# Kernel tuning notes

Measured on AMD Instinct MI355X. Metric: run time of the kernel, lower is better.

## Reference

```python
import jax, jax.numpy as jnp
import numpy as np

N = 16384      # instances (cells) per bag
IN = 2000      # input_dim (genes)
E1, E2 = 1024, 512   # encoder_dims
HID = 512      # hidden_dim
NH, HD = 8, 64 # num_heads, head_dim
LK = 256       # linformer_k
EPROJ_N = 10000  # fixed in-dim of E/F projections
NEXP, MH = 4, 256  # moe experts, moe hidden (= classifier_dims[0])
C1, C2, NC = 256, 128, 2


def _ln(x, g, b):
    m = jnp.mean(x, axis=-1, keepdims=True)
    v = jnp.var(x, axis=-1, keepdims=True)
    return (x - m) * jax.lax.rsqrt(v + 1e-5) * g + b


def setup_inputs() -> dict:
    key = jax.random.key(0)
    ks = jax.random.split(key, 24)
    s = 0.02
    f32 = jnp.float32
    inp = {
        'x': jax.random.normal(ks[0], (N, IN), dtype=f32),
        'enc_w1': jax.random.normal(ks[1], (IN, E1), dtype=f32) * s,
        'enc_b1': jnp.zeros((E1,), f32),
        'enc_w2': jax.random.normal(ks[2], (E1, E2), dtype=f32) * s,
        'enc_b2': jnp.zeros((E2,), f32),
        'enc_w3': jax.random.normal(ks[3], (E2, HID), dtype=f32) * s,
        'enc_b3': jnp.zeros((HID,), f32),
        'q_w': jax.random.normal(ks[4], (HID, HID), dtype=f32) * s,
        'q_b': jnp.zeros((HID,), f32),
        'k_w': jax.random.normal(ks[5], (HID, HID), dtype=f32) * s,
        'k_b': jnp.zeros((HID,), f32),
        'v_w': jax.random.normal(ks[6], (HID, HID), dtype=f32) * s,
        'v_b': jnp.zeros((HID,), f32),
        'o_w': jax.random.normal(ks[7], (HID, HID), dtype=f32) * s,
        'o_b': jnp.zeros((HID,), f32),
        'E_w': jax.random.normal(ks[8], (LK, EPROJ_N), dtype=f32) * s,  # nn.Linear(10000, k).weight
        'F_w': jax.random.normal(ks[9], (LK, EPROJ_N), dtype=f32) * s,
        'ln1_g': jnp.ones((HID,), f32), 'ln1_b': jnp.zeros((HID,), f32),
        'ln2_g': jnp.ones((HID,), f32), 'ln2_b': jnp.zeros((HID,), f32),
        'gate_w': jax.random.normal(ks[10], (HID, NEXP), dtype=f32) * s,
        'gate_b': jnp.zeros((NEXP,), f32),
        'moe_w1': jax.random.normal(ks[11], (NEXP, HID, MH), dtype=f32) * s,
        'moe_b1': jnp.zeros((NEXP, MH), f32),
        'moe_w2': jax.random.normal(ks[12], (NEXP, MH), dtype=f32) * s,
        'moe_b2': jnp.zeros((NEXP,), f32),
        'cls_w1': jax.random.normal(ks[13], (HID, C1), dtype=f32) * s,
        'cls_b1': jnp.zeros((C1,), f32),
        'cls_w2': jax.random.normal(ks[14], (C1, C2), dtype=f32) * s,
        'cls_b2': jnp.zeros((C2,), f32),
        'cls_w3': jax.random.normal(ks[15], (C2, NC), dtype=f32) * s,
        'cls_b3': jnp.zeros((NC,), f32),
    }
    return inp


def reference(x, enc_w1, enc_b1, enc_w2, enc_b2, enc_w3, enc_b3,
              q_w, q_b, k_w, k_b, v_w, v_b, o_w, o_b, E_w, F_w,
              ln1_g, ln1_b, ln2_g, ln2_b,
              gate_w, gate_b, moe_w1, moe_b1, moe_w2, moe_b2,
              cls_w1, cls_b1, cls_w2, cls_b2, cls_w3, cls_b3):
    # --- instance encoder (chunking in torch is math-equivalent to one pass) ---
    h = jax.nn.relu(x @ enc_w1 + enc_b1)
    h = jax.nn.relu(h @ enc_w2 + enc_b2)
    feat = jax.nn.relu(h @ enc_w3 + enc_b3)          # [N, HID]
    # dropouts / InstanceDropout are identity at inference

    # --- linformer attention (single bag, batch of 1) ---
    Q = (feat @ q_w + q_b).reshape(N, NH, HD).transpose(1, 0, 2)  # [H, N, D]
    K = (feat @ k_w + k_b).reshape(N, NH, HD).transpose(1, 0, 2)
    V = (feat @ v_w + v_b).reshape(N, NH, HD).transpose(1, 0, 2)
    # N > linformer_k and the torch inner check (seq_len <= weight.size(0)=LK)
    # is false, so E/F are bilinearly resized from [10000, LK] to [LK, N], then
    # transposed to [N, LK] (matches F.interpolate align_corners=False).
    E_m = jax.image.resize(E_w.T, (LK, N), method='bilinear').T   # [N, LK]
    F_m = jax.image.resize(F_w.T, (LK, N), method='bilinear').T   # [N, LK]
    Kc = jnp.einsum('hnd,nk->hkd', K, E_m)           # [H, LK, D]
    Vc = jnp.einsum('hnd,nk->hkd', V, F_m)           # [H, LK, D]
    scores = jax.nn.softmax(jnp.einsum('hnd,hkd->hnk', Q, Kc) * (HD ** -0.5), axis=-1)
    ao = jnp.einsum('hnk,hkd->hnd', scores, Vc)      # [H, N, D]
    attn_out = ao.transpose(1, 0, 2).reshape(N, HID) @ o_w + o_b

    att = _ln(attn_out + feat, ln1_g, ln1_b)
    att = _ln(att, ln2_g, ln2_b)                     # [N, HID]

    # --- MoE MIL aggregation: gated mixture of per-expert attention pooling ---
    gates = jax.nn.softmax(jnp.mean(att, axis=0) @ gate_w + gate_b)       # [E]
    Hm = jnp.tanh(jnp.einsum('nd,edh->enh', att, moe_w1) + moe_b1[:, None, :])
    sc = jnp.einsum('enh,eh->en', Hm, moe_w2) + moe_b2[:, None]           # [E, N]
    a = jax.nn.softmax(sc, axis=1)                   # per-expert instance attention
    attn_weights = gates @ a                         # [N]
    bag = attn_weights @ att                         # [HID]

    # --- classifier ---
    c = jax.nn.relu(bag @ cls_w1 + cls_b1)
    c = jax.nn.relu(c @ cls_w2 + cls_b2)
    disease = c @ cls_w3 + cls_b3                    # [NC]
    # use_domain_adaptation=False -> no domain output
    return (bag, disease, attn_weights)
```

## Files before the change

### kernel.cpp

```cpp
#include <hip/hip_runtime.h>

#define DI __device__ __forceinline__

DI float bf2f(unsigned short u){ unsigned int v = ((unsigned int)u)<<16; float f; __builtin_memcpy(&f,&v,4); return f; }
DI unsigned short f2bf(float f){ unsigned int v; __builtin_memcpy(&v,&f,4); v = v + 0x7FFFu + ((v>>16)&1u); return (unsigned short)(v>>16); }

typedef __attribute__((ext_vector_type(8))) short bf16x8;
typedef __attribute__((ext_vector_type(4))) float f32x4;

#define GLD_LDS16(src, dst) __builtin_amdgcn_global_load_lds( \
    (const __attribute__((address_space(1))) void*)(src), \
    (__attribute__((address_space(3))) void*)(dst), 16, 0, 0)

DI void barrier_() { asm volatile("" ::: "memory"); __builtin_amdgcn_s_barrier(); asm volatile("" ::: "memory"); }

template<int ACT>
__global__ __launch_bounds__(256) void gemm2_k(
    const unsigned short* __restrict__ A, const unsigned short* __restrict__ Bt,
    const float* __restrict__ bias, unsigned short* __restrict__ C,
    int K, int lda, int ldb, int ldc)
{
  __shared__ unsigned short As[8192];
  __shared__ unsigned short Bs[8192];
  const int tid = threadIdx.x, lane = tid & 63, wid = tid >> 6;
  const int wm = wid >> 1, wn = wid & 1;
  const int nx = gridDim.x;
  const int bid = blockIdx.x + nx*blockIdx.y;
  const int cpx = (nx*gridDim.y) >> 3;
  const int wg = (bid & 7)*cpx + (bid >> 3);
  const long long mBase = (long long)(wg / nx) << 7;
  const long long nBase = (long long)(wg % nx) << 7;
  const int q = lane >> 4, r15 = lane & 15;

  f32x4 acc[4][4];
#pragma unroll
  for (int i=0;i<4;i++)
#pragma unroll
    for (int j=0;j<4;j++)
#pragma unroll
      for (int r=0;r<4;r++) acc[i][j][r] = 0.f;

  const int nkt = K >> 6;
  for (int kt=0; kt<nkt; ++kt) {
    const int k0 = kt << 6;
#pragma unroll
    for (int it=0; it<4; ++it) {
      const int dbase = (it<<8) + (wid<<6);
      const int d = dbase + lane;
      const int row = d >> 3, cc = d & 7, sc = cc ^ (row & 7);
      GLD_LDS16(A + (mBase + row)*(long long)lda + k0 + (sc<<3), As + (dbase<<3));
      GLD_LDS16(Bt + (nBase + row)*(long long)ldb + k0 + (sc<<3), Bs + (dbase<<3));
    }
    __syncthreads();
#pragma unroll
    for (int ks=0; ks<2; ++ks) {
      bf16x8 af[4], bfr[4];
#pragma unroll
      for (int mi=0; mi<4; ++mi) {
        const int row = (wm<<6) + (mi<<4) + r15;
        const int ch = ((ks<<2)+q) ^ (row&7);
        af[mi] = *(const bf16x8*)(As + (row<<6) + (ch<<3));
      }
#pragma unroll
      for (int ni=0; ni<4; ++ni) {
        const int col = (wn<<6) + (ni<<4) + r15;
        const int ch = ((ks<<2)+q) ^ (col&7);
        bfr[ni] = *(const bf16x8*)(Bs + (col<<6) + (ch<<3));
      }
#pragma unroll
      for (int mi=0; mi<4; ++mi)
#pragma unroll
        for (int ni=0; ni<4; ++ni)
          acc[mi][ni] = __builtin_amdgcn_mfma_f32_16x16x32_bf16(af[mi], bfr[ni], acc[mi][ni], 0, 0, 0);
    }
    __syncthreads();
  }
#pragma unroll
  for (int ni=0; ni<4; ++ni) {
    const long long n = nBase + (wn<<6) + (ni<<4) + r15;
    const float bval = bias[n];
#pragma unroll
    for (int mi=0; mi<4; ++mi) {
#pragma unroll
      for (int r=0; r<4; ++r) {
        const long long m = mBase + (wm<<6) + (mi<<4) + (q<<2) + r;
        float v = acc[mi][ni][r] + bval;
        if constexpr (ACT==1) v = fmaxf(v, 0.f);
        C[m*(long long)ldc + n] = f2bf(v);
      }
    }
  }
}

template<int ACT, bool MOE>
__global__ __launch_bounds__(512,2) void gemm4_k(
    const unsigned short* __restrict__ A, const unsigned short* __restrict__ Bt,
    const float* __restrict__ bias, unsigned short* __restrict__ C,
    const float* __restrict__ w2, float* __restrict__ scp,
    int K, int lda, int ldb, int ldc)
{
  __shared__ unsigned short As[2][16384];
  __shared__ unsigned short Bs[2][16384];
  const int tid = threadIdx.x, lane = tid & 63, wid = tid >> 6;
  const int wm = wid >> 2, wn = wid & 3;
  const int q = lane >> 4, r15 = lane & 15;
  const int nx = gridDim.x;
  const int bid = blockIdx.x + nx*blockIdx.y;
  const int cpx = (nx*gridDim.y) >> 3;
  const int wg = (bid & 7)*cpx + (bid >> 3);
  const long long mBase = (long long)(wg / nx) << 8;
  const long long nBase = (long long)(wg % nx) << 8;

  f32x4 acc[8][4];
#pragma unroll
  for (int i=0;i<8;i++)
#pragma unroll
    for (int j=0;j<4;j++)
#pragma unroll
      for (int r=0;r<4;r++) acc[i][j][r] = 0.f;

  const int NT = K >> 6;

#define G4_STA(j, nb, kk) { const int d_ = tid + ((j)<<9); const int row_ = d_>>3, c_ = d_&7, sc_ = c_ ^ (row_&7); \
    GLD_LDS16(A + (mBase+row_)*(long long)lda + (kk) + (sc_<<3), &As[nb][d_<<3]); }
#define G4_STB(j, nb, kk) { const int d_ = tid + ((j)<<9); const int row_ = d_>>3, c_ = d_&7, sc_ = c_ ^ (row_&7); \
    GLD_LDS16(Bt + (nBase+row_)*(long long)ldb + (kk) + (sc_<<3), &Bs[nb][d_<<3]); }

  G4_STB(0,0,0); G4_STB(1,0,0); G4_STB(2,0,0); G4_STB(3,0,0);
  G4_STA(0,0,0); G4_STA(2,0,0); G4_STA(1,0,0); G4_STA(3,0,0);

  for (int t=0; t<NT; ++t) {
    const int b = t & 1, nb = b ^ 1;
    const bool more = (t+1 < NT);
    const int k1 = (t+1) << 6;
    bf16x8 aF[8], bL[4], bH[4];

    asm volatile("s_waitcnt vmcnt(2)" ::: "memory");
    barrier_();
#pragma unroll
    for (int mi=0; mi<4; ++mi)
#pragma unroll
      for (int ks=0; ks<2; ++ks) {
        const int row = (wm<<7) + (mi<<4) + r15;
        const int ch = ((ks<<2)+q) ^ (row&7);
        aF[mi*2+ks] = *(const bf16x8*)&As[b][(row<<6) + (ch<<3)];
      }
#pragma unroll
    for (int ni=0; ni<2; ++ni)
#pragma unroll
      for (int ks=0; ks<2; ++ks) {
        const int col = (wn<<6) + (ni<<4) + r15;
        const int ch = ((ks<<2)+q) ^ (col&7);
        bL[ni*2+ks] = *(const bf16x8*)&Bs[b][(col<<6) + (ch<<3)];
      }
    if (more) { G4_STB(0,nb,k1); G4_STB(1,nb,k1); }
    __builtin_amdgcn_s_setprio(1);
#pragma unroll
    for (int mi=0; mi<4; ++mi)
#pragma unroll
      for (int ni=0; ni<2; ++ni)
#pragma unroll
        for (int ks=0; ks<2; ++ks)
          acc[mi][ni] = __builtin_amdgcn_mfma_f32_16x16x32_bf16(aF[mi*2+ks], bL[ni*2+ks], acc[mi][ni], 0,0,0);
    __builtin_amdgcn_s_setprio(0);
    barrier_();

#pragma unroll
    for (int ni=0; ni<2; ++ni)
#pragma unroll
      for (int ks=0; ks<2; ++ks) {
        const int col = (wn<<6) + ((ni+2)<<4) + r15;
        const int ch = ((ks<<2)+q) ^ (col&7);
        bH[ni*2+ks] = *(const bf16x8*)&Bs[b][(col<<6) + (ch<<3)];
      }
    if (more) { G4_STB(2,nb,k1); G4_STB(3,nb,k1); }
    __builtin_amdgcn_s_setprio(1);
#pragma unroll
    for (int mi=0; mi<4; ++mi)
#pragma unroll
      for (int ni=0; ni<2; ++ni)
#pragma unroll
        for (int ks=0; ks<2; ++ks)
          acc[mi][ni+2] = __builtin_amdgcn_mfma_f32_16x16x32_bf16(aF[mi*2+ks], bH[ni*2+ks], acc[mi][ni+2], 0,0,0);
    __builtin_amdgcn_s_setprio(0);
    barrier_();

    if (more) { asm volatile("s_waitcnt vmcnt(4)" ::: "memory"); }
    else      { asm volatile("s_waitcnt vmcnt(0)" ::: "memory"); }
    barrier_();
#pragma unroll
    for (int mi=0; mi<4; ++mi)
#pragma unroll
      for (int ks=0; ks<2; ++ks) {
        const int row = (wm<<7) + ((mi+4)<<4) + r15;
        const int ch = ((ks<<2)+q) ^ (row&7);
        aF[mi*2+ks] = *(const bf16x8*)&As[b][(row<<6) + (ch<<3)];
      }
    if (more) { G4_STA(0,nb,k1); G4_STA(2,nb,k1); }
    __builtin_amdgcn_s_setprio(1);
#pragma unroll
    for (int mi=0; mi<4; ++mi)
#pragma unroll
      for (int ni=0; ni<2; ++ni)
#pragma unroll
        for (int ks=0; ks<2; ++ks)
          acc[mi+4][ni] = __builtin_amdgcn_mfma_f32_16x16x32_bf16(aF[mi*2+ks], bL[ni*2+ks], acc[mi+4][ni], 0,0,0);
    __builtin_amdgcn_s_setprio(0);
    barrier_();

    if (more) { G4_STA(1,nb,k1); G4_STA(3,nb,k1); }
    __builtin_amdgcn_s_setprio(1);
#pragma unroll
    for (int mi=0; mi<4; ++mi)
#pragma unroll
      for (int ni=0; ni<2; ++ni)
#pragma unroll
        for (int ks=0; ks<2; ++ks)
          acc[mi+4][ni+2] = __builtin_amdgcn_mfma_f32_16x16x32_bf16(aF[mi*2+ks], bH[ni*2+ks], acc[mi+4][ni+2], 0,0,0);
    __builtin_amdgcn_s_setprio(0);
    barrier_();
  }
#undef G4_STA
#undef G4_STB

  if constexpr (MOE) {
    const int e = (int)(nBase >> 8);
#pragma unroll
    for (int mi=0; mi<8; ++mi) {
#pragma unroll
      for (int r=0; r<4; ++r) {
        float p = 0.f;
#pragma unroll
        for (int ni=0; ni<4; ++ni) {
          const int n = (int)nBase + (wn<<6) + (ni<<4) + r15;
          const float v = acc[mi][ni][r] + bias[n];
          const float th = 1.f - 2.f/(__expf(2.f*v) + 1.f);
          p += th * w2[n];
        }
        p += __shfl_xor(p,1,64); p += __shfl_xor(p,2,64);
        p += __shfl_xor(p,4,64); p += __shfl_xor(p,8,64);
        if (r15 == 0) {
          const long long m = mBase + (wm<<7) + (mi<<4) + (q<<2) + r;
          atomicAdd(scp + ((long long)e<<14) + m, p);
        }
      }
    }
  } else {
#pragma unroll
    for (int ni=0; ni<4; ++ni) {
      const long long n = nBase + (wn<<6) + (ni<<4) + r15;
      const float bval = bias[n];
#pragma unroll
      for (int mi=0; mi<8; ++mi) {
#pragma unroll
        for (int r=0; r<4; ++r) {
          const long long m = mBase + (wm<<7) + (mi<<4) + (q<<2) + r;
          float v = acc[mi][ni][r] + bval;
          if constexpr (ACT==1) v = fmaxf(v, 0.f);
          C[m*(long long)ldc + n] = f2bf(v);
        }
      }
    }
  }
}

__global__ __launch_bounds__(256) void cvtx_k(const float* __restrict__ x, unsigned short* __restrict__ xb)
{
  const long long id = (long long)blockIdx.x*256 + threadIdx.x;
  const long long row = id >> 8; const int c = (int)(id & 255);
  bf16x8 v;
  if (c < 250) {
    const float* p = x + row*2000 + c*8;
    const float4 f0 = *(const float4*)p, f1 = *(const float4*)(p+4);
    v[0]=(short)f2bf(f0.x); v[1]=(short)f2bf(f0.y); v[2]=(short)f2bf(f0.z); v[3]=(short)f2bf(f0.w);
    v[4]=(short)f2bf(f1.x); v[5]=(short)f2bf(f1.y); v[6]=(short)f2bf(f1.z); v[7]=(short)f2bf(f1.w);
  } else {
#pragma unroll
    for (int j=0;j<8;j++) v[j]=0;
  }
  *(bf16x8*)(xb + (id<<3)) = v;
}

__global__ __launch_bounds__(256) void cvtw_k(const float* __restrict__ B, unsigned short* __restrict__ Bt,
    int K, int N, int Kpad, long long bszi, long long bszo)
{
  __shared__ float tile[64][65];
  const float* Bz = B + (long long)blockIdx.z*bszi;
  unsigned short* Bo = Bt + (long long)blockIdx.z*bszo;
  const int k0 = blockIdx.x<<6, n0 = blockIdx.y<<6;
  const int c = threadIdx.x & 63, rg = threadIdx.x >> 6;
#pragma unroll
  for (int j=0;j<16;j++){
    const int r = (j<<2) + rg;
    const int k = k0 + r;
    tile[r][c] = (k < K) ? Bz[(long long)k*N + n0 + c] : 0.f;
  }
  __syncthreads();
#pragma unroll
  for (int j=0;j<16;j++){
    const int nn = (j<<2) + rg;
    Bo[(long long)(n0+nn)*Kpad + k0 + c] = f2bf(tile[c][nn]);
  }
}

__global__ __launch_bounds__(256) void cvtw5_k(
    const float* __restrict__ s0, const float* __restrict__ s1, const float* __restrict__ s2,
    const float* __restrict__ s3, const float* __restrict__ s4,
    unsigned short* __restrict__ d0, unsigned short* __restrict__ d1, unsigned short* __restrict__ d2,
    unsigned short* __restrict__ d3, unsigned short* __restrict__ d4)
{
  __shared__ float tile[64][65];
  const int z = blockIdx.z;
  const float* Bz = (z==0)?s0:(z==1)?s1:(z==2)?s2:(z==3)?s3:s4;
  unsigned short* Bo = (z==0)?d0:(z==1)?d1:(z==2)?d2:(z==3)?d3:d4;
  const int k0 = blockIdx.x<<6, n0 = blockIdx.y<<6;
  const int c = threadIdx.x & 63, rg = threadIdx.x >> 6;
#pragma unroll
  for (int j=0;j<16;j++){
    const int r = (j<<2) + rg;
    tile[r][c] = Bz[(long long)(k0+r)*512 + n0 + c];
  }
  __syncthreads();
#pragma unroll
  for (int j=0;j<16;j++){
    const int nn = (j<<2) + rg;
    Bo[(long long)(n0+nn)*512 + k0 + c] = f2bf(tile[c][nn]);
  }
}

__global__ __launch_bounds__(256) void t1cat_k(const float* __restrict__ Ew, const float* __restrict__ Fw,
    float* __restrict__ t1, const float* __restrict__ qb, const float* __restrict__ kb,
    const float* __restrict__ vb, float* __restrict__ qkvb)
{
  const int k = blockIdx.x, which = blockIdx.y, c = threadIdx.x;
  if (which == 0 && k < 3) {
    const float* src = (k==0) ? qb : (k==1) ? kb : vb;
    qkvb[k*512 + c]       = src[c];
    qkvb[k*512 + 256 + c] = src[256 + c];
  }
  const float* W = which ? Fw : Ew;
  const float ksc = 39.0625f;
  const float inv = 1.f/39.0625f;
  const float sf = (k + 0.5f)*ksc - 0.5f;
  int ilo = (int)ceilf(sf - ksc); if (ilo < 0) ilo = 0;
  int ihi = (int)floorf(sf + ksc); if (ihi > 9999) ihi = 9999;
  float acc = 0.f, wsum = 0.f;
  for (int i=ilo; i<=ihi; ++i) {
    const float w = 1.f - fabsf(sf - (float)i)*inv;
    if (w > 0.f) { acc += w * W[c*10000 + i]; wsum += w; }
  }
  t1[(which*256 + k)*256 + c] = acc / wsum;
}

__global__ __launch_bounds__(512) void red_k(const unsigned short* __restrict__ qkv,
                                             float* __restrict__ red)
{
  const int c = blockIdx.x, which = blockIdx.y, j = threadIdx.x;
  const unsigned short* X = qkv + (which ? 1024 : 512);
  int nlo = 64*c - 32; if (nlo < 0) nlo = 0;
  int nhi = 64*c + 95; if (nhi > 16383) nhi = 16383;
  float acc = 0.f;
  for (int n=nlo; n<=nhi; ++n) {
    float sf = (n + 0.5f)*0.015625f - 0.5f;
    sf = fminf(fmaxf(sf, 0.f), 255.f);
    const int c0 = (int)sf;
    const float f = sf - (float)c0;
    float w = 0.f;
    if (c == c0) w = 1.f - f;
    else if (c == c0+1) w = f;
    if (w != 0.f) acc += w * bf2f(X[(long long)n*1536 + j]);
  }
  red[(which*256 + c)*512 + j] = acc;
}

__global__ __launch_bounds__(512) void kc_k(const float* __restrict__ t1, const float* __restrict__ red,
                                            unsigned short* __restrict__ Kc, unsigned short* __restrict__ Vct)
{
  const int k = blockIdx.x, which = blockIdx.y, j = threadIdx.x;
  const float* T = t1 + (which*256 + k)*256;
  const float* R = red + which*131072;
  float acc = 0.f;
  for (int c=0; c<256; ++c) acc += T[c] * R[c*512 + j];
  const int h = j >> 6, d = j & 63;
  if (which == 0) Kc [(h<<14) + (k<<6) + d] = f2bf(acc);
  else            Vct[(h<<14) + (d<<8) + k] = f2bf(acc);
}

__global__ __launch_bounds__(256) void attn_k(
    const unsigned short* __restrict__ Qg, const unsigned short* __restrict__ Kc,
    const unsigned short* __restrict__ Vct, unsigned short* __restrict__ ao)
{
  __shared__ unsigned short Ks[16384];
  __shared__ unsigned short Vs[16384];
  __shared__ unsigned short Ps[32768];
  const int h = blockIdx.y;
  const long long mBase = (long long)blockIdx.x << 7;
  const int tid = threadIdx.x, lane = tid & 63, wid = tid >> 6;
  const int q = lane >> 4, r15 = lane & 15;

#pragma unroll
  for (int it=0; it<8; ++it) {
    const int dbase = (it<<8) + (wid<<6);
    const int d = dbase + lane;
    {
      const int row = d >> 3, cc = d & 7, sc = cc ^ (row & 7);
      GLD_LDS16(Kc + (h<<14) + (row<<6) + (sc<<3), Ks + (dbase<<3));
    }
    {
      const int row = d >> 5, cc = d & 31, sc = (cc & 24) | ((cc ^ (row & 7)) & 7);
      GLD_LDS16(Vct + (h<<14) + (row<<8) + (sc<<3), Vs + (dbase<<3));
    }
  }
  __syncthreads();

  f32x4 acc[2][16];
#pragma unroll
  for (int mi=0;mi<2;mi++)
#pragma unroll
    for (int ni=0;ni<16;ni++)
#pragma unroll
      for (int r=0;r<4;r++) acc[mi][ni][r] = 0.f;

#pragma unroll
  for (int ks=0; ks<2; ++ks) {
    bf16x8 af[2];
#pragma unroll
    for (int mi=0; mi<2; ++mi) {
      const long long m = mBase + (wid<<5) + (mi<<4) + r15;
      af[mi] = *(const bf16x8*)(Qg + m*1536 + (h<<6) + (ks<<5) + (q<<3));
    }
#pragma unroll
    for (int ni=0; ni<16; ++ni) {
      const int col = (ni<<4) + r15;
      const int ch = ((ks<<2)+q) ^ (col&7);
      const bf16x8 bv = *(const bf16x8*)(Ks + (col<<6) + (ch<<3));
      acc[0][ni] = __builtin_amdgcn_mfma_f32_16x16x32_bf16(af[0], bv, acc[0][ni], 0,0,0);
      acc[1][ni] = __builtin_amdgcn_mfma_f32_16x16x32_bf16(af[1], bv, acc[1][ni], 0,0,0);
    }
  }

#pragma unroll
  for (int mi=0; mi<2; ++mi) {
#pragma unroll
    for (int r=0; r<4; ++r) {
      float mx = -3.4e38f;
#pragma unroll
      for (int ni=0; ni<16; ++ni) mx = fmaxf(mx, acc[mi][ni][r]);
      mx = fmaxf(mx, __shfl_xor(mx,1,64)); mx = fmaxf(mx, __shfl_xor(mx,2,64));
      mx = fmaxf(mx, __shfl_xor(mx,4,64)); mx = fmaxf(mx, __shfl_xor(mx,8,64));
      float s = 0.f;
#pragma unroll
      for (int ni=0; ni<16; ++ni) {
        const float e = __expf((acc[mi][ni][r] - mx)*0.125f);
        acc[mi][ni][r] = e; s += e;
      }
      s += __shfl_xor(s,1,64); s += __shfl_xor(s,2,64);
      s += __shfl_xor(s,4,64); s += __shfl_xor(s,8,64);
      const float inv = 1.f / s;
      const int row = (wid<<5) + (mi<<4) + (q<<2) + r;
#pragma unroll
      for (int ni=0; ni<16; ++ni) {
        const int col = (ni<<4) + r15;
        const int ch = col >> 3;
        const int chs = (ch & 24) | ((ch ^ (row & 7)) & 7);
        Ps[(row<<8) + (chs<<3) + (col&7)] = f2bf(acc[mi][ni][r]*inv);
      }
    }
  }
  __syncthreads();

  f32x4 o[2][4];
#pragma unroll
  for (int mi=0;mi<2;mi++)
#pragma unroll
    for (int ni=0;ni<4;ni++)
#pragma unroll
      for (int r=0;r<4;r++) o[mi][ni][r] = 0.f;

#pragma unroll
  for (int kk=0; kk<8; ++kk) {
    bf16x8 pa[2];
#pragma unroll
    for (int mi=0; mi<2; ++mi) {
      const int row = (wid<<5) + (mi<<4) + r15;
      const int ch = (kk<<2) + q;
      const int chs = (ch & 24) | ((ch ^ (row & 7)) & 7);
      pa[mi] = *(const bf16x8*)(Ps + (row<<8) + (chs<<3));
    }
#pragma unroll
    for (int ni=0; ni<4; ++ni) {
      const int vrow = (ni<<4) + r15;
      const int ch = (kk<<2) + q;
      const int chs = (ch & 24) | ((ch ^ (vrow & 7)) & 7);
      const bf16x8 bv = *(const bf16x8*)(Vs + (vrow<<8) + (chs<<3));
      o[0][ni] = __builtin_amdgcn_mfma_f32_16x16x32_bf16(pa[0], bv, o[0][ni], 0,0,0);
      o[1][ni] = __builtin_amdgcn_mfma_f32_16x16x32_bf16(pa[1], bv, o[1][ni], 0,0,0);
    }
  }
#pragma unroll
  for (int mi=0; mi<2; ++mi)
#pragma unroll
    for (int ni=0; ni<4; ++ni)
#pragma unroll
      for (int r=0; r<4; ++r) {
        const long long m = mBase + (wid<<5) + (mi<<4) + (q<<2) + r;
        ao[m*512 + (h<<6) + (ni<<4) + r15] = f2bf(o[mi][ni][r]);
      }
}

__global__ __launch_bounds__(256) void ln2_k(
    const unsigned short* __restrict__ x1b, const unsigned short* __restrict__ x2b,
    const float* __restrict__ g1, const float* __restrict__ b1,
    const float* __restrict__ g2, const float* __restrict__ b2,
    unsigned short* __restrict__ out)
{
  __shared__ float sred[8];
  const int tid = threadIdx.x, lane = tid & 63, wid = tid >> 6;
  const long long base = (long long)blockIdx.x << 9;
  const float x0 = bf2f(x1b[base+tid])     + bf2f(x2b[base+tid]);
  const float x1 = bf2f(x1b[base+256+tid]) + bf2f(x2b[base+256+tid]);
  float s = x0+x1, qq = x0*x0 + x1*x1;
#pragma unroll
  for (int o=32;o;o>>=1){ s += __shfl_xor(s,o,64); qq += __shfl_xor(qq,o,64); }
  if (lane==0){ sred[wid]=s; sred[4+wid]=qq; }
  __syncthreads();
  float mean = (sred[0]+sred[1]+sred[2]+sred[3]) * (1.f/512.f);
  float var  = (sred[4]+sred[5]+sred[6]+sred[7]) * (1.f/512.f) - mean*mean;
  float rs = rsqrtf(var + 1e-5f);
  const float y0 = (x0-mean)*rs*g1[tid]     + b1[tid];
  const float y1 = (x1-mean)*rs*g1[tid+256] + b1[tid+256];
  __syncthreads();
  s = y0+y1; qq = y0*y0 + y1*y1;
#pragma unroll
  for (int o=32;o;o>>=1){ s += __shfl_xor(s,o,64); qq += __shfl_xor(qq,o,64); }
  if (lane==0){ sred[wid]=s; sred[4+wid]=qq; }
  __syncthreads();
  mean = (sred[0]+sred[1]+sred[2]+sred[3]) * (1.f/512.f);
  var  = (sred[4]+sred[5]+sred[6]+sred[7]) * (1.f/512.f) - mean*mean;
  rs = rsqrtf(var + 1e-5f);
  out[base+tid]     = f2bf((y0-mean)*rs*g2[tid]     + b2[tid]);
  out[base+256+tid] = f2bf((y1-mean)*rs*g2[tid+256] + b2[tid+256]);
}

__global__ __launch_bounds__(256) void wcolsum_k(const unsigned short* __restrict__ att,
                                                 float* __restrict__ part, float* __restrict__ zf)
{
  const int c = threadIdx.x;
  if (zf) { zf[((long long)blockIdx.x<<9)+c] = 0.f; zf[((long long)blockIdx.x<<9)+c+256] = 0.f; }
  const long long r0 = (long long)blockIdx.x * 128;
  float a0=0.f, a1=0.f;
  for (int r=0;r<128;r++){
    const unsigned short* p = att + ((r0+r)<<9);
    a0 += bf2f(p[c]); a1 += bf2f(p[c+256]);
  }
  part[((long long)blockIdx.x<<9)+c]     = a0;
  part[((long long)blockIdx.x<<9)+c+256] = a1;
}

__global__ __launch_bounds__(512) void meangates_k(const float* __restrict__ part,
    const float* __restrict__ gw, const float* __restrict__ gb, float* __restrict__ gates)
{
  __shared__ float mv[512];
  __shared__ float tmp[4];
  const int t = threadIdx.x;
  float s = 0.f;
  for (int b=0;b<128;b++) s += part[(b<<9)+t];
  mv[t] = s * (1.f/16384.f);
  __syncthreads();
  if (t < 4) {
    float a = gb[t];
    for (int d=0; d<512; ++d) a += mv[d]*gw[d*4+t];
    tmp[t] = a;
  }
  __syncthreads();
  if (t == 0) {
    const float m = fmaxf(fmaxf(tmp[0],tmp[1]),fmaxf(tmp[2],tmp[3]));
    float e[4]; float ss=0.f;
    for (int i=0;i<4;i++){ e[i]=__expf(tmp[i]-m); ss+=e[i]; }
    for (int i=0;i<4;i++) gates[i] = e[i]/ss;
  }
}

__global__ __launch_bounds__(1024) void moestat_k(const float* __restrict__ sc,
                                                  float* __restrict__ mstat, float* __restrict__ sstat)
{
  __shared__ float red[1024];
  const int e = blockIdx.x, t = threadIdx.x;
  const float* p = sc + e*16384;
  float m = -3.4e38f;
  for (int n=t; n<16384; n+=1024) m = fmaxf(m, p[n]);
  red[t] = m; __syncthreads();
  for (int o=512;o;o>>=1){ if (t<o) red[t]=fmaxf(red[t],red[t+o]); __syncthreads(); }
  m = red[0]; __syncthreads();
  float s = 0.f;
  for (int n=t; n<16384; n+=1024) s += __expf(p[n]-m);
  red[t] = s; __syncthreads();
  for (int o=512;o;o>>=1){ if (t<o) red[t]+=red[t+o]; __syncthreads(); }
  if (t==0){ mstat[e]=m; sstat[e]=red[0]; }
}

__global__ __launch_bounds__(256) void wbag_k(const unsigned short* __restrict__ att,
    const float* __restrict__ scp, const float* __restrict__ gates,
    const float* __restrict__ mstat, const float* __restrict__ sstat,
    float* __restrict__ part, float* __restrict__ dout)
{
  __shared__ float wrow[128];
  const int c = threadIdx.x;
  const long long r0 = (long long)blockIdx.x * 128;
  if (c < 128) {
    const long long n = r0 + c;
    float w = 0.f;
#pragma unroll
    for (int e=0;e<4;e++) w += gates[e]*__expf(scp[((long long)e<<14)+n]-mstat[e]) / sstat[e];
    wrow[c] = w;
    dout[514 + n] = w;
  }
  __syncthreads();
  float a0=0.f, a1=0.f;
  for (int r=0;r<128;r++){
    const float w = wrow[r];
    const unsigned short* p = att + ((r0+r)<<9);
    a0 += w*bf2f(p[c]); a1 += w*bf2f(p[c+256]);
  }
  part[((long long)blockIdx.x<<9)+c]     = a0;
  part[((long long)blockIdx.x<<9)+c+256] = a1;
}

__global__ __launch_bounds__(512) void cls2_k(const float* __restrict__ bagp,
    const float* __restrict__ w1, const float* __restrict__ b1,
    const float* __restrict__ w2, const float* __restrict__ b2,
    const float* __restrict__ w3, const float* __restrict__ b3, float* __restrict__ dout)
{
  __shared__ float bag[512]; __shared__ float c1[256]; __shared__ float c2[128];
  const int tid = threadIdx.x;
  float s = 0.f;
  for (int b=0;b<128;b++) s += bagp[(b<<9)+tid];
  bag[tid] = s; dout[tid] = s;
  __syncthreads();
  if (tid < 256) {
    float a = b1[tid];
    for (int d=0; d<512; ++d) a += bag[d]*w1[d*256+tid];
    c1[tid] = fmaxf(a, 0.f);
  }
  __syncthreads();
  if (tid < 128) {
    float a2 = b2[tid];
    for (int d=0; d<256; ++d) a2 += c1[d]*w2[d*128+tid];
    c2[tid] = fmaxf(a2, 0.f);
  }
  __syncthreads();
  if (tid < 2) {
    float a3 = b3[tid];
    for (int d=0; d<128; ++d) a3 += c2[d]*w3[d*2+tid];
    dout[512 + tid] = a3;
  }
}

extern "C" void kernel_launch(void* const* d_in, const int* in_sizes, int n_in,
                              void* d_out, int out_size, void* d_ws, size_t ws_size,
                              hipStream_t stream)
{
  (void)in_sizes; (void)n_in; (void)out_size; (void)ws_size;
  const float* x      = (const float*)d_in[0];
  const float* enc_w1 = (const float*)d_in[1];
  const float* enc_b1 = (const float*)d_in[2];
  const float* enc_w2 = (const float*)d_in[3];
  const float* enc_b2 = (const float*)d_in[4];
  const float* enc_w3 = (const float*)d_in[5];
  const float* enc_b3 = (const float*)d_in[6];
  const float* q_w    = (const float*)d_in[7];
  const float* q_b    = (const float*)d_in[8];
  const float* k_w    = (const float*)d_in[9];
  const float* k_b    = (const float*)d_in[10];
  const float* v_w    = (const float*)d_in[11];
  const float* v_b    = (const float*)d_in[12];
  const float* o_w    = (const float*)d_in[13];
  const float* o_b    = (const float*)d_in[14];
  const float* E_w    = (const float*)d_in[15];
  const float* F_w    = (const float*)d_in[16];
  const float* ln1_g  = (const float*)d_in[17];
  const float* ln1_b  = (const float*)d_in[18];
  const float* ln2_g  = (const float*)d_in[19];
  const float* ln2_b  = (const float*)d_in[20];
  const float* gate_w = (const float*)d_in[21];
  const float* gate_b = (const float*)d_in[22];
  const float* moe_w1 = (const float*)d_in[23];
  const float* moe_b1 = (const float*)d_in[24];
  const float* moe_w2 = (const float*)d_in[25];
  const float* cls_w1 = (const float*)d_in[27];
  const float* cls_b1 = (const float*)d_in[28];
  const float* cls_w2 = (const float*)d_in[29];
  const float* cls_b2 = (const float*)d_in[30];
  const float* cls_w3 = (const float*)d_in[31];
  const float* cls_b3 = (const float*)d_in[32];

  char* ws = (char*)d_ws;
  const size_t MB = 1024*1024;
  unsigned short* x_bf  = (unsigned short*)(ws + 0);
  unsigned short* h1    = (unsigned short*)(ws + 64*MB);
  unsigned short* h2    = (unsigned short*)(ws + 0);
  unsigned short* feat  = (unsigned short*)(ws + 16*MB);
  unsigned short* qkv   = (unsigned short*)(ws + 32*MB);
  unsigned short* ao    = (unsigned short*)(ws + 80*MB);
  unsigned short* attno = (unsigned short*)(ws + 0);
  unsigned short* att   = (unsigned short*)(ws + 96*MB);
  unsigned short* w1t   = (unsigned short*)(ws + 112*MB);
  unsigned short* w2t   = (unsigned short*)(ws + 116*MB);
  unsigned short* w3t   = (unsigned short*)(ws + 117*MB);
  unsigned short* qkvw  = (unsigned short*)(ws + 117*MB + 512*1024);
  unsigned short* owt   = (unsigned short*)(ws + 119*MB);
  unsigned short* mwt   = (unsigned short*)(ws + 119*MB + 512*1024);
  float*  t1b   = (float*)(ws + 120*MB + 512*1024);
  float*  redb  = (float*)(ws + 121*MB);
  unsigned short* Kcbf  = (unsigned short*)(ws + 122*MB);
  unsigned short* Vctbf = (unsigned short*)(ws + 122*MB + 256*1024);
  float*  colp  = (float*)(ws + 122*MB + 512*1024);
  float*  bagp  = (float*)(ws + 122*MB + 768*1024);
  float*  qkvb  = (float*)(ws + 123*MB);
  float*  gatesp= (float*)(ws + 123*MB + 8192);
  float*  scp   = (float*)(ws + 123*MB + 16384);
  float*  mstat = (float*)(ws + 123*MB + 16384 + 262144);
  float*  sstat = (float*)(ws + 123*MB + 16384 + 262144 + 64);
  float*  dout  = (float*)d_out;

  cvtx_k<<<16384,256,0,stream>>>(x, x_bf);
  cvtw_k<<<dim3(32,16,1),256,0,stream>>>(enc_w1, w1t, 2000,1024,2048, 0,0);
  cvtw_k<<<dim3(16, 8,1),256,0,stream>>>(enc_w2, w2t, 1024, 512,1024, 0,0);
  cvtw5_k<<<dim3(8,8,5),256,0,stream>>>(enc_w3, q_w, k_w, v_w, o_w,
                                        w3t, qkvw, qkvw + 512*512, qkvw + 1024*512, owt);
  cvtw_k<<<dim3( 8, 4,4),256,0,stream>>>(moe_w1, mwt, 512, 256, 512, 512*256, 256*512);
  t1cat_k<<<dim3(256,2),256,0,stream>>>(E_w, F_w, t1b, q_b, k_b, v_b, qkvb);

  gemm4_k<1,false><<<dim3(4,64,1),512,0,stream>>>(x_bf, w1t, enc_b1, h1, nullptr,nullptr, 2048,2048,2048,1024);
  gemm2_k<1><<<dim3(4,128,1),256,0,stream>>>(h1, w2t, enc_b2, h2,   1024,1024,1024, 512);
  gemm2_k<1><<<dim3(4,128,1),256,0,stream>>>(h2, w3t, enc_b3, feat,  512, 512, 512, 512);
  gemm4_k<0,false><<<dim3(6,64,1),512,0,stream>>>(feat, qkvw, qkvb, qkv, nullptr,nullptr, 512,512,512,1536);
  red_k<<<dim3(256,2),512,0,stream>>>(qkv, redb);
  kc_k <<<dim3(256,2),512,0,stream>>>(t1b, redb, Kcbf, Vctbf);
  attn_k<<<dim3(128,8),256,0,stream>>>(qkv, Kcbf, Vctbf, ao);
  gemm2_k<0><<<dim3(4,128,1),256,0,stream>>>(ao, owt, o_b, attno, 512,512,512,512);
  ln2_k<<<16384,256,0,stream>>>(attno, feat, ln1_g, ln1_b, ln2_g, ln2_b, att);
  wcolsum_k<<<128,256,0,stream>>>(att, colp, scp);
  meangates_k<<<1,512,0,stream>>>(colp, gate_w, gate_b, gatesp);
  gemm4_k<0,true><<<dim3(4,64,1),512,0,stream>>>(att, mwt, moe_b1, nullptr, moe_w2, scp, 512,512,512,0);
  moestat_k<<<4,1024,0,stream>>>(scp, mstat, sstat);
  wbag_k<<<128,256,0,stream>>>(att, scp, gatesp, mstat, sstat, bagp, dout);
  cls2_k<<<1,512,0,stream>>>(bagp, cls_w1, cls_b1, cls_w2, cls_b2, cls_w3, cls_b3, dout);
}
```

Baseline: 496.8 us.

## Fuse prep kernels, fuse layernorm with column sums, drop gemm4 barriers

Merges the input conversion, weight transposes and E/F interpolation into one prep launch, cutting several kernel launches. Replaces the per-row double layernorm and the separate column-sum kernel with one kernel that handles 64 rows per block and also writes column partials and zeroes the score buffer. It also removes two barriers from the gemm4 main loop to reduce synchronisation. Removing those barriers risks LDS race conditions between the MFMA fragment reads and the asynchronous global-to-LDS loads of the next tile.

```diff
diff --git a/kernel.cpp b/kernel.cpp
--- a/kernel.cpp
+++ b/kernel.cpp
@@ -183,7 +183,6 @@
         for (int ks=0; ks<2; ++ks)
           acc[mi][ni+2] = __builtin_amdgcn_mfma_f32_16x16x32_bf16(aF[mi*2+ks], bH[ni*2+ks], acc[mi][ni+2], 0,0,0);
     __builtin_amdgcn_s_setprio(0);
-    barrier_();
 
     if (more) { asm volatile("s_waitcnt vmcnt(4)" ::: "memory"); }
     else      { asm volatile("s_waitcnt vmcnt(0)" ::: "memory"); }
@@ -218,7 +217,6 @@
         for (int ks=0; ks<2; ++ks)
           acc[mi+4][ni+2] = __builtin_amdgcn_mfma_f32_16x16x32_bf16(aF[mi*2+ks], bH[ni*2+ks], acc[mi+4][ni+2], 0,0,0);
     __builtin_amdgcn_s_setprio(0);
-    barrier_();
   }
 #undef G4_STA
 #undef G4_STB
@@ -264,92 +262,93 @@
   }
 }
 
-__global__ __launch_bounds__(256) void cvtx_k(const float* __restrict__ x, unsigned short* __restrict__ xb)
-{
-  const long long id = (long long)blockIdx.x*256 + threadIdx.x;
-  const long long row = id >> 8; const int c = (int)(id & 255);
-  bf16x8 v;
-  if (c < 250) {
-    const float* p = x + row*2000 + c*8;
-    const float4 f0 = *(const float4*)p, f1 = *(const float4*)(p+4);
-    v[0]=(short)f2bf(f0.x); v[1]=(short)f2bf(f0.y); v[2]=(short)f2bf(f0.z); v[3]=(short)f2bf(f0.w);
-    v[4]=(short)f2bf(f1.x); v[5]=(short)f2bf(f1.y); v[6]=(short)f2bf(f1.z); v[7]=(short)f2bf(f1.w);
-  } else {
-#pragma unroll
-    for (int j=0;j<8;j++) v[j]=0;
-  }
-  *(bf16x8*)(xb + (id<<3)) = v;
-}
-
-__global__ __launch_bounds__(256) void cvtw_k(const float* __restrict__ B, unsigned short* __restrict__ Bt,
-    int K, int N, int Kpad, long long bszi, long long bszo)
-{
-  __shared__ float tile[64][65];
-  const float* Bz = B + (long long)blockIdx.z*bszi;
-  unsigned short* Bo = Bt + (long long)blockIdx.z*bszo;
-  const int k0 = blockIdx.x<<6, n0 = blockIdx.y<<6;
-  const int c = threadIdx.x & 63, rg = threadIdx.x >> 6;
+DI void transpose64(const float* __restrict__ src, unsigned short* __restrict__ dst,
+                    int K, int N, int Kpad, int k0, int n0, float (*tile)[65], int tid)
+{
+  const int c = tid & 63, rg = tid >> 6;
 #pragma unroll
   for (int j=0;j<16;j++){
     const int r = (j<<2) + rg;
     const int k = k0 + r;
-    tile[r][c] = (k < K) ? Bz[(long long)k*N + n0 + c] : 0.f;
+    tile[r][c] = (k < K) ? src[(long long)k*N + n0 + c] : 0.f;
   }
   __syncthreads();
 #pragma unroll
   for (int j=0;j<16;j++){
     const int nn = (j<<2) + rg;
-    Bo[(long long)(n0+nn)*Kpad + k0 + c] = f2bf(tile[c][nn]);
-  }
-}
-
-__global__ __launch_bounds__(256) void cvtw5_k(
-    const float* __restrict__ s0, const float* __restrict__ s1, const float* __restrict__ s2,
-    const float* __restrict__ s3, const float* __restrict__ s4,
-    unsigned short* __restrict__ d0, unsigned short* __restrict__ d1, unsigned short* __restrict__ d2,
-    unsigned short* __restrict__ d3, unsigned short* __restrict__ d4)
+    dst[(long long)(n0+nn)*Kpad + k0 + c] = f2bf(tile[c][nn]);
+  }
+}
+
+__global__ __launch_bounds__(256) void prep_k(
+    const float* __restrict__ x, unsigned short* __restrict__ xb,
+    const float* __restrict__ enc_w1, unsigned short* __restrict__ w1t,
+    const float* __restrict__ enc_w2, unsigned short* __restrict__ w2t,
+    const float* __restrict__ enc_w3, const float* __restrict__ q_w,
+    const float* __restrict__ k_w, const float* __restrict__ v_w, const float* __restrict__ o_w,
+    unsigned short* __restrict__ w3t, unsigned short* __restrict__ qkvw, unsigned short* __restrict__ owt,
+    const float* __restrict__ moe_w1, unsigned short* __restrict__ mwt,
+    const float* __restrict__ Ew, const float* __restrict__ Fw, float* __restrict__ t1,
+    const float* __restrict__ qb, const float* __restrict__ kb, const float* __restrict__ vb,
+    float* __restrict__ qkvb)
 {
   __shared__ float tile[64][65];
-  const int z = blockIdx.z;
-  const float* Bz = (z==0)?s0:(z==1)?s1:(z==2)?s2:(z==3)?s3:s4;
-  unsigned short* Bo = (z==0)?d0:(z==1)?d1:(z==2)?d2:(z==3)?d3:d4;
-  const int k0 = blockIdx.x<<6, n0 = blockIdx.y<<6;
-  const int c = threadIdx.x & 63, rg = threadIdx.x >> 6;
-#pragma unroll
-  for (int j=0;j<16;j++){
-    const int r = (j<<2) + rg;
-    tile[r][c] = Bz[(long long)(k0+r)*512 + n0 + c];
-  }
-  __syncthreads();
-#pragma unroll
-  for (int j=0;j<16;j++){
-    const int nn = (j<<2) + rg;
-    Bo[(long long)(n0+nn)*512 + k0 + c] = f2bf(tile[c][nn]);
-  }
-}
-
-__global__ __launch_bounds__(256) void t1cat_k(const float* __restrict__ Ew, const float* __restrict__ Fw,
-    float* __restrict__ t1, const float* __restrict__ qb, const float* __restrict__ kb,
-    const float* __restrict__ vb, float* __restrict__ qkvb)
-{
-  const int k = blockIdx.x, which = blockIdx.y, c = threadIdx.x;
-  if (which == 0 && k < 3) {
-    const float* src = (k==0) ? qb : (k==1) ? kb : vb;
-    qkvb[k*512 + c]       = src[c];
-    qkvb[k*512 + 256 + c] = src[256 + c];
-  }
-  const float* W = which ? Fw : Ew;
-  const float ksc = 39.0625f;
-  const float inv = 1.f/39.0625f;
-  const float sf = (k + 0.5f)*ksc - 0.5f;
-  int ilo = (int)ceilf(sf - ksc); if (ilo < 0) ilo = 0;
-  int ihi = (int)floorf(sf + ksc); if (ihi > 9999) ihi = 9999;
-  float acc = 0.f, wsum = 0.f;
-  for (int i=ilo; i<=ihi; ++i) {
-    const float w = 1.f - fabsf(sf - (float)i)*inv;
-    if (w > 0.f) { acc += w * W[c*10000 + i]; wsum += w; }
-  }
-  t1[(which*256 + k)*256 + c] = acc / wsum;
+  const int b = blockIdx.x, tid = threadIdx.x;
+  if (b < 4096) {
+#pragma unroll
+    for (int i=0;i<4;i++){
+      const long long cid = (long long)b*1024 + i*256 + tid;
+      const long long row = cid >> 8; const int c = (int)(cid & 255);
+      bf16x8 v;
+      if (c < 250) {
+        const float* p = x + row*2000 + c*8;
+        const float4 f0 = *(const float4*)p, f1 = *(const float4*)(p+4);
+        v[0]=(short)f2bf(f0.x); v[1]=(short)f2bf(f0.y); v[2]=(short)f2bf(f0.z); v[3]=(short)f2bf(f0.w);
+        v[4]=(short)f2bf(f1.x); v[5]=(short)f2bf(f1.y); v[6]=(short)f2bf(f1.z); v[7]=(short)f2bf(f1.w);
+      } else {
+#pragma unroll
+        for (int j=0;j<8;j++) v[j]=0;
+      }
+      *(bf16x8*)(xb + (cid<<3)) = v;
+    }
+  } else if (b < 4608) {
+    const int bb = b - 4096;
+    transpose64(enc_w1, w1t, 2000, 1024, 2048, (bb&31)<<6, (bb>>5)<<6, tile, tid);
+  } else if (b < 4736) {
+    const int bb = b - 4608;
+    transpose64(enc_w2, w2t, 1024, 512, 1024, (bb&15)<<6, (bb>>4)<<6, tile, tid);
+  } else if (b < 5056) {
+    const int bb = b - 4736;
+    const int z = bb >> 6, r = bb & 63;
+    const float* s = (z==0)?enc_w3:(z==1)?q_w:(z==2)?k_w:(z==3)?v_w:o_w;
+    unsigned short* d = (z==0)?w3t:(z==1)?qkvw:(z==2)?(qkvw+512*512):(z==3)?(qkvw+1024*512):owt;
+    transpose64(s, d, 512, 512, 512, (r&7)<<6, (r>>3)<<6, tile, tid);
+  } else if (b < 5184) {
+    const int bb = b - 5056;
+    const int z = bb >> 5, r = bb & 31;
+    transpose64(moe_w1 + (long long)z*512*256, mwt + (long long)z*256*512,
+                512, 256, 512, (r&7)<<6, (r>>3)<<6, tile, tid);
+  } else {
+    const int bb = b - 5184;
+    const int k = bb & 255, which = bb >> 8, c = tid;
+    if (which == 0 && k < 3) {
+      const float* src = (k==0) ? qb : (k==1) ? kb : vb;
+      qkvb[k*512 + c]       = src[c];
+      qkvb[k*512 + 256 + c] = src[256 + c];
+    }
+    const float* W = which ? Fw : Ew;
+    const float ksc = 39.0625f;
+    const float inv = 1.f/39.0625f;
+    const float sf = (k + 0.5f)*ksc - 0.5f;
+    int ilo = (int)ceilf(sf - ksc); if (ilo < 0) ilo = 0;
+    int ihi = (int)floorf(sf + ksc); if (ihi > 9999) ihi = 9999;
+    float acc = 0.f, wsum = 0.f;
+    for (int i=ilo; i<=ihi; ++i) {
+      const float w = 1.f - fabsf(sf - (float)i)*inv;
+      if (w > 0.f) { acc += w * W[c*10000 + i]; wsum += w; }
+    }
+    t1[(which*256 + k)*256 + c] = acc / wsum;
+  }
 }
 
 __global__ __launch_bounds__(512) void red_k(const unsigned short* __restrict__ qkv,
@@ -508,53 +507,54 @@
       }
 }
 
-__global__ __launch_bounds__(256) void ln2_k(
-    const unsigned short* __restrict__ x1b, const unsigned short* __restrict__ x2b,
+__global__ __launch_bounds__(256) void ln64_k(
+    const unsigned short* __restrict__ attno, const unsigned short* __restrict__ feat,
     const float* __restrict__ g1, const float* __restrict__ b1,
     const float* __restrict__ g2, const float* __restrict__ b2,
-    unsigned short* __restrict__ out)
-{
-  __shared__ float sred[8];
+    unsigned short* __restrict__ att, float* __restrict__ colp, float* __restrict__ scp)
+{
+  __shared__ float cred[4][512];
   const int tid = threadIdx.x, lane = tid & 63, wid = tid >> 6;
-  const long long base = (long long)blockIdx.x << 9;
-  const float x0 = bf2f(x1b[base+tid])     + bf2f(x2b[base+tid]);
-  const float x1 = bf2f(x1b[base+256+tid]) + bf2f(x2b[base+256+tid]);
-  float s = x0+x1, qq = x0*x0 + x1*x1;
-#pragma unroll
-  for (int o=32;o;o>>=1){ s += __shfl_xor(s,o,64); qq += __shfl_xor(qq,o,64); }
-  if (lane==0){ sred[wid]=s; sred[4+wid]=qq; }
-  __syncthreads();
-  float mean = (sred[0]+sred[1]+sred[2]+sred[3]) * (1.f/512.f);
-  float var  = (sred[4]+sred[5]+sred[6]+sred[7]) * (1.f/512.f) - mean*mean;
-  float rs = rsqrtf(var + 1e-5f);
-  const float y0 = (x0-mean)*rs*g1[tid]     + b1[tid];
-  const float y1 = (x1-mean)*rs*g1[tid+256] + b1[tid+256];
-  __syncthreads();
-  s = y0+y1; qq = y0*y0 + y1*y1;
-#pragma unroll
-  for (int o=32;o;o>>=1){ s += __shfl_xor(s,o,64); qq += __shfl_xor(qq,o,64); }
-  if (lane==0){ sred[wid]=s; sred[4+wid]=qq; }
-  __syncthreads();
-  mean = (sred[0]+sred[1]+sred[2]+sred[3]) * (1.f/512.f);
-  var  = (sred[4]+sred[5]+sred[6]+sred[7]) * (1.f/512.f) - mean*mean;
-  rs = rsqrtf(var + 1e-5f);
-  out[base+tid]     = f2bf((y0-mean)*rs*g2[tid]     + b2[tid]);
-  out[base+256+tid] = f2bf((y1-mean)*rs*g2[tid+256] + b2[tid+256]);
-}
-
-__global__ __launch_bounds__(256) void wcolsum_k(const unsigned short* __restrict__ att,
-                                                 float* __restrict__ part, float* __restrict__ zf)
-{
-  const int c = threadIdx.x;
-  if (zf) { zf[((long long)blockIdx.x<<9)+c] = 0.f; zf[((long long)blockIdx.x<<9)+c+256] = 0.f; }
-  const long long r0 = (long long)blockIdx.x * 128;
-  float a0=0.f, a1=0.f;
-  for (int r=0;r<128;r++){
-    const unsigned short* p = att + ((r0+r)<<9);
-    a0 += bf2f(p[c]); a1 += bf2f(p[c+256]);
-  }
-  part[((long long)blockIdx.x<<9)+c]     = a0;
-  part[((long long)blockIdx.x<<9)+c+256] = a1;
+  const int c0 = lane << 3;
+  scp[((long long)blockIdx.x<<8) + tid] = 0.f;
+  float g1v[8], b1v[8], g2v[8], b2v[8];
+#pragma unroll
+  for (int j=0;j<8;j++){ g1v[j]=g1[c0+j]; b1v[j]=b1[c0+j]; g2v[j]=g2[c0+j]; b2v[j]=b2[c0+j]; }
+  float cacc[8];
+#pragma unroll
+  for (int j=0;j<8;j++) cacc[j]=0.f;
+  for (int rr=0; rr<16; ++rr) {
+    const long long row = ((long long)blockIdx.x<<6) + (rr<<2) + wid;
+    const bf16x8 a = *(const bf16x8*)(attno + (row<<9) + c0);
+    const bf16x8 f = *(const bf16x8*)(feat  + (row<<9) + c0);
+    float xv[8]; float s=0.f, qs=0.f;
+#pragma unroll
+    for (int j=0;j<8;j++){ xv[j] = bf2f((unsigned short)a[j]) + bf2f((unsigned short)f[j]); s += xv[j]; qs += xv[j]*xv[j]; }
+#pragma unroll
+    for (int o=32;o;o>>=1){ s += __shfl_xor(s,o,64); qs += __shfl_xor(qs,o,64); }
+    float m = s*(1.f/512.f);
+    float rs = rsqrtf(qs*(1.f/512.f) - m*m + 1e-5f);
+    float y[8]; s=0.f; qs=0.f;
+#pragma unroll
+    for (int j=0;j<8;j++){ y[j] = (xv[j]-m)*rs*g1v[j] + b1v[j]; s += y[j]; qs += y[j]*y[j]; }
+#pragma unroll
+    for (int o=32;o;o>>=1){ s += __shfl_xor(s,o,64); qs += __shfl_xor(qs,o,64); }
+    m = s*(1.f/512.f);
+    rs = rsqrtf(qs*(1.f/512.f) - m*m + 1e-5f);
+    bf16x8 ov;
+#pragma unroll
+    for (int j=0;j<8;j++){ const float z = (y[j]-m)*rs*g2v[j] + b2v[j]; cacc[j] += z; ov[j] = (short)f2bf(z); }
+    *(bf16x8*)(att + (row<<9) + c0) = ov;
+  }
+#pragma unroll
+  for (int j=0;j<8;j++) cred[wid][c0+j] = cacc[j];
+  __syncthreads();
+  {
+    const float v0 = cred[0][tid]+cred[1][tid]+cred[2][tid]+cred[3][tid];
+    const float v1 = cred[0][tid+256]+cred[1][tid+256]+cred[2][tid+256]+cred[3][tid+256];
+    colp[((long long)blockIdx.x<<9)+tid]     = v0;
+    colp[((long long)blockIdx.x<<9)+tid+256] = v1;
+  }
 }
 
 __global__ __launch_bounds__(512) void meangates_k(const float* __restrict__ part,
@@ -564,7 +564,7 @@
   __shared__ float tmp[4];
   const int t = threadIdx.x;
   float s = 0.f;
-  for (int b=0;b<128;b++) s += part[(b<<9)+t];
+  for (int b=0;b<256;b++) s += part[(b<<9)+t];
   mv[t] = s * (1.f/16384.f);
   __syncthreads();
   if (t < 4) {
@@ -715,21 +715,17 @@
   unsigned short* Kcbf  = (unsigned short*)(ws + 122*MB);
   unsigned short* Vctbf = (unsigned short*)(ws + 122*MB + 256*1024);
   float*  colp  = (float*)(ws + 122*MB + 512*1024);
-  float*  bagp  = (float*)(ws + 122*MB + 768*1024);
-  float*  qkvb  = (float*)(ws + 123*MB);
-  float*  gatesp= (float*)(ws + 123*MB + 8192);
-  float*  scp   = (float*)(ws + 123*MB + 16384);
-  float*  mstat = (float*)(ws + 123*MB + 16384 + 262144);
-  float*  sstat = (float*)(ws + 123*MB + 16384 + 262144 + 64);
+  float*  bagp  = (float*)(ws + 123*MB);
+  float*  qkvb  = (float*)(ws + 123*MB + 256*1024);
+  float*  gatesp= (float*)(ws + 123*MB + 264*1024);
+  float*  scp   = (float*)(ws + 123*MB + 268*1024);
+  float*  mstat = (float*)(ws + 123*MB + 524*1024);
+  float*  sstat = (float*)(ws + 123*MB + 524*1024 + 64);
   float*  dout  = (float*)d_out;
 
-  cvtx_k<<<16384,256,0,stream>>>(x, x_bf);
-  cvtw_k<<<dim3(32,16,1),256,0,stream>>>(enc_w1, w1t, 2000,1024,2048, 0,0);
-  cvtw_k<<<dim3(16, 8,1),256,0,stream>>>(enc_w2, w2t, 1024, 512,1024, 0,0);
-  cvtw5_k<<<dim3(8,8,5),256,0,stream>>>(enc_w3, q_w, k_w, v_w, o_w,
-                                        w3t, qkvw, qkvw + 512*512, qkvw + 1024*512, owt);
-  cvtw_k<<<dim3( 8, 4,4),256,0,stream>>>(moe_w1, mwt, 512, 256, 512, 512*256, 256*512);
-  t1cat_k<<<dim3(256,2),256,0,stream>>>(E_w, F_w, t1b, q_b, k_b, v_b, qkvb);
+  prep_k<<<5696,256,0,stream>>>(x, x_bf, enc_w1, w1t, enc_w2, w2t,
+                                enc_w3, q_w, k_w, v_w, o_w, w3t, qkvw, owt,
+                                moe_w1, mwt, E_w, F_w, t1b, q_b, k_b, v_b, qkvb);
 
   gemm4_k<1,false><<<dim3(4,64,1),512,0,stream>>>(x_bf, w1t, enc_b1, h1, nullptr,nullptr, 2048,2048,2048,1024);
   gemm2_k<1><<<dim3(4,128,1),256,0,stream>>>(h1, w2t, enc_b2, h2,   1024,1024,1024, 512);
@@ -739,8 +735,7 @@
   kc_k <<<dim3(256,2),512,0,stream>>>(t1b, redb, Kcbf, Vctbf);
   attn_k<<<dim3(128,8),256,0,stream>>>(qkv, Kcbf, Vctbf, ao);
   gemm2_k<0><<<dim3(4,128,1),256,0,stream>>>(ao, owt, o_b, attno, 512,512,512,512);
-  ln2_k<<<16384,256,0,stream>>>(attno, feat, ln1_g, ln1_b, ln2_g, ln2_b, att);
-  wcolsum_k<<<128,256,0,stream>>>(att, colp, scp);
+  ln64_k<<<256,256,0,stream>>>(attno, feat, ln1_g, ln1_b, ln2_g, ln2_b, att, colp, scp);
   meangates_k<<<1,512,0,stream>>>(colp, gate_w, gate_b, gatesp);
   gemm4_k<0,true><<<dim3(4,64,1),512,0,stream>>>(att, mwt, moe_b1, nullptr, moe_w2, scp, 512,512,512,0);
   moestat_k<<<4,1024,0,stream>>>(scp, mstat, sstat);
```

Result: faster. 473.8 us (-4.6%).
